# Optimization experiments

Hardware: AMD Instinct MI355X
Metric: run time of the kernel (lower is better)

Reference implementation:

```python
import jax, jax.numpy as jnp
import numpy as np

NEG_INF = -1.0e9


def _gru_cell(x, h, W_ih, W_hh, b_ih, b_hh):
    # torch GRU gate order: reset, update, new
    gi = x @ W_ih.T + b_ih          # [B, 3H]
    gh = h @ W_hh.T + b_hh          # [B, 3H]
    i_r, i_z, i_n = jnp.split(gi, 3, axis=-1)
    h_r, h_z, h_n = jnp.split(gh, 3, axis=-1)
    r = jax.nn.sigmoid(i_r + h_r)
    z = jax.nn.sigmoid(i_z + h_z)
    ng = jnp.tanh(i_n + r * h_n)
    return (1.0 - z) * ng + z * h


def setup_inputs() -> dict:
    key = jax.random.key(0)
    n, H, B = 512, 512, 256
    ks = jax.random.split(key, 10)
    s_ih0 = 1.0 / np.sqrt(n)
    s = 1.0 / np.sqrt(H)
    return {
        "batch_size": B,
        "W_ih0": jax.random.normal(ks[0], (3 * H, n), jnp.float32) * s_ih0,
        "W_hh0": jax.random.normal(ks[1], (3 * H, H), jnp.float32) * s,
        "b_ih0": jax.random.normal(ks[2], (3 * H,), jnp.float32) * s,
        "b_hh0": jax.random.normal(ks[3], (3 * H,), jnp.float32) * s,
        "W_ih1": jax.random.normal(ks[4], (3 * H, H), jnp.float32) * s,
        "W_hh1": jax.random.normal(ks[5], (3 * H, H), jnp.float32) * s,
        "b_ih1": jax.random.normal(ks[6], (3 * H,), jnp.float32) * s,
        "b_hh1": jax.random.normal(ks[7], (3 * H,), jnp.float32) * s,
        "W_out": jax.random.normal(ks[8], (n, H), jnp.float32) * s,
        "b_out": jax.random.normal(ks[9], (n,), jnp.float32) * s,
    }


def reference(batch_size, W_ih0, W_hh0, b_ih0, b_hh0,
              W_ih1, W_hh1, b_ih1, b_hh1, W_out, b_out):
    n = W_out.shape[0]
    H = W_out.shape[1]
    B = batch_size

    h0 = jnp.zeros((B, H), jnp.float32)
    h1 = jnp.zeros((B, H), jnp.float32)
    available = jnp.ones((B, n), jnp.bool_)
    inp = jnp.ones((B, n), jnp.float32)
    log_probs = jnp.zeros((B,), jnp.float32)

    step_keys = jax.random.split(jax.random.key(42), n)

    def step(carry, key):
        h0, h1, available, inp, lp = carry
        h0n = _gru_cell(inp, h0, W_ih0, W_hh0, b_ih0, b_hh0)
        h1n = _gru_cell(h0n, h1, W_ih1, W_hh1, b_ih1, b_hh1)
        logits = h1n @ W_out.T + b_out                       # [B, n]
        logits = jnp.where(available, logits, NEG_INF)
        probs = jax.nn.softmax(logits, axis=-1)
        idx = jax.random.categorical(key, logits, axis=-1)   # ~ multinomial(probs)
        p_sel = jnp.take_along_axis(probs, idx[:, None], axis=1)[:, 0]
        lp = lp + jnp.log(p_sel + 1e-9)
        oh = jax.nn.one_hot(idx, n, dtype=jnp.float32)       # row of perm matrix
        available = available & ~jax.nn.one_hot(idx, n, dtype=jnp.bool_)
        return (h0n, h1n, available, oh, lp), oh

    (h0, h1, available, inp, log_probs), rows = jax.lax.scan(
        step, (h0, h1, available, inp, log_probs), step_keys)
    perm_matrix = jnp.transpose(rows, (1, 0, 2))             # [B, n, n]
    return perm_matrix, log_probs
```

## Files before the change

### kernel.cpp

```cpp
#include <hip/hip_runtime.h>
#include <cstdint>
#include <cstddef>

#define BB 256
#define NN 512
#define HH 512
#define G3 1536

typedef short bf16x8 __attribute__((ext_vector_type(8)));
typedef float f32x4 __attribute__((ext_vector_type(4)));

__device__ __align__(16) short g_Whh0[2 * 786432];
__device__ __align__(16) short g_Whh1[2 * 786432];
__device__ __align__(16) short g_Wih1[2 * 786432];
__device__ __align__(16) short g_Wout[2 * 262144];
__device__ __align__(16) short g_h0p[2][2 * 131072];
__device__ __align__(16) short g_h1p[2][2 * 131072];
__device__ __align__(16) float g_h0f[BB * HH];
__device__ __align__(16) float g_h1f[BB * HH];
__device__ __align__(16) float g_gh1[BB * G3];
__device__ __align__(16) float g_logits[2][BB * NN];
__device__ __align__(16) float g_gum[2][BB * NN];
__device__ __align__(16) float g_WihT[NN * G3];
__device__ __align__(16) float g_ones[G3];
__device__ float g_lp[BB];
__device__ unsigned g_avail[2][BB * 16];
__device__ int g_idx[BB];

__device__ __forceinline__ unsigned short bf16_rne(float f) {
  uint32_t u = __float_as_uint(f);
  uint32_t r = u + 0x7FFFu + ((u >> 16) & 1u);
  return (unsigned short)(r >> 16);
}
__device__ __forceinline__ float bf16_to_f(unsigned short h) {
  return __uint_as_float(((uint32_t)h) << 16);
}
__device__ __forceinline__ float sigf(float x) {
  return 1.0f / (1.0f + expf(-x));
}
__device__ __forceinline__ f32x4 mfma16(bf16x8 a, bf16x8 b, f32x4 c) {
  return __builtin_amdgcn_mfma_f32_16x16x32_bf16(a, b, c, 0, 0, 0);
}

__device__ __forceinline__ uint32_t rotl32(uint32_t v, int r) {
  return (v << r) | (v >> (32 - r));
}
__device__ __forceinline__ void threefry2x32(uint32_t k0, uint32_t k1,
                                             uint32_t x0, uint32_t x1,
                                             uint32_t& o0, uint32_t& o1) {
  uint32_t k2 = k0 ^ k1 ^ 0x1BD11BDAu;
  x0 += k0; x1 += k1;
  x0 += x1; x1 = rotl32(x1, 13); x1 ^= x0;
  x0 += x1; x1 = rotl32(x1, 15); x1 ^= x0;
  x0 += x1; x1 = rotl32(x1, 26); x1 ^= x0;
  x0 += x1; x1 = rotl32(x1, 6);  x1 ^= x0;
  x0 += k1; x1 += k2 + 1u;
  x0 += x1; x1 = rotl32(x1, 17); x1 ^= x0;
  x0 += x1; x1 = rotl32(x1, 29); x1 ^= x0;
  x0 += x1; x1 = rotl32(x1, 16); x1 ^= x0;
  x0 += x1; x1 = rotl32(x1, 24); x1 ^= x0;
  x0 += k2; x1 += k0 + 2u;
  x0 += x1; x1 = rotl32(x1, 13); x1 ^= x0;
  x0 += x1; x1 = rotl32(x1, 15); x1 ^= x0;
  x0 += x1; x1 = rotl32(x1, 26); x1 ^= x0;
  x0 += x1; x1 = rotl32(x1, 6);  x1 ^= x0;
  x0 += k0; x1 += k1 + 3u;
  x0 += x1; x1 = rotl32(x1, 17); x1 ^= x0;
  x0 += x1; x1 = rotl32(x1, 29); x1 ^= x0;
  x0 += x1; x1 = rotl32(x1, 16); x1 ^= x0;
  x0 += x1; x1 = rotl32(x1, 24); x1 ^= x0;
  x0 += k1; x1 += k2 + 4u;
  x0 += x1; x1 = rotl32(x1, 13); x1 ^= x0;
  x0 += x1; x1 = rotl32(x1, 15); x1 ^= x0;
  x0 += x1; x1 = rotl32(x1, 26); x1 ^= x0;
  x0 += x1; x1 = rotl32(x1, 6);  x1 ^= x0;
  x0 += k2; x1 += k0 + 5u;
  o0 = x0; o1 = x1;
}

__device__ __forceinline__ float gumbel_from_bits(uint32_t bits) {
  float u = __uint_as_float((bits >> 9) | 0x3f800000u) - 1.0f;
  if (u == 0.0f) u = 1.17549435e-38f;
  return -logf(-logf(u));
}

__global__ __launch_bounds__(256) void init_state_kernel() {
  int i = blockIdx.x * 256 + threadIdx.x;
  if (i < BB * HH) { g_h0f[i] = 0.0f; g_h1f[i] = 0.0f; }
  if (i < 262144) {
    ((uint32_t*)g_h0p)[i] = 0u;
    ((uint32_t*)g_h1p)[i] = 0u;
  }
  if (i < 2 * BB * 16) ((unsigned*)g_avail)[i] = 0xFFFFFFFFu;
  if (i < BB) { g_lp[i] = 0.0f; g_idx[i] = 0; }
}

__global__ __launch_bounds__(256) void ones_row_kernel(
    const float* __restrict__ W_ih0, const float* __restrict__ b_ih0) {
  int j = blockIdx.x * 256 + threadIdx.x;
  if (j < G3) {
    const float* row = W_ih0 + (size_t)j * NN;
    float s = 0.0f;
    for (int k = 0; k < NN; ++k) s += row[k];
    g_ones[j] = s + b_ih0[j];
  }
}

__global__ __launch_bounds__(256) void transpose_kernel(
    const float* __restrict__ in) {
  __shared__ float tile[32][33];
  int bx = blockIdx.x;
  int by = blockIdx.y;
  int tx = threadIdx.x & 31;
  int ty = threadIdx.x >> 5;
  for (int i = 0; i < 32; i += 8)
    tile[ty + i][tx] = in[(size_t)(by * 32 + ty + i) * NN + bx * 32 + tx];
  __syncthreads();
  for (int i = 0; i < 32; i += 8)
    g_WihT[(size_t)(bx * 32 + ty + i) * G3 + by * 32 + tx] = tile[tx][ty + i];
}

__global__ __launch_bounds__(256) void split_kernel(
    const float* __restrict__ W, short* __restrict__ dst, int rows,
    int plane) {
  int i = blockIdx.x * 256 + threadIdx.x;
  if (i >= rows * 64) return;
  int c = i >> 6;
  int jb = i & 63;
  int ci = c & 15;
  int tile = (rows == G3) ? (((c & 511) >> 4) * 3 + (c >> 9)) : (c >> 4);
  int S = jb >> 2, qu = jb & 3;
  int off = (tile * 16 + S) * 512 + qu * 128 + ci * 8;
  const float* src = W + (size_t)c * 512 + jb * 8;
  float v[8];
  *(float4*)v = *(const float4*)src;
  *(float4*)(v + 4) = *(const float4*)(src + 4);
  short hb[8], lb[8];
#pragma unroll
  for (int e = 0; e < 8; ++e) {
    unsigned short h = bf16_rne(v[e]);
    hb[e] = (short)h;
    lb[e] = (short)bf16_rne(v[e] - bf16_to_f(h));
  }
  *(bf16x8*)(dst + off) = *(const bf16x8*)hb;
  *(bf16x8*)(dst + plane + off) = *(const bf16x8*)lb;
}

__global__ __launch_bounds__(256) void k0_sample(
    int t, const float* __restrict__ b_out, float* __restrict__ out_perm,
    float* __restrict__ out_lp) {
  const int mt = blockIdx.x;
  const int tid = threadIdx.x;
  if (t < NN) {
    float* lz = g_logits[t & 1] + mt * 16 * NN;
    for (int i = tid; i < 16 * NN; i += 256) lz[i] = 0.0f;
  }
  if (t == 0) return;
  const int tp = t - 1;
  const int rr = tid >> 4, l16 = tid & 15;
  const int b = mt * 16 + rr;
  const float* lrow = g_logits[tp & 1] + b * NN;
  const float* grow = g_gum[tp & 1] + b * NN;
  unsigned aw = g_avail[tp & 1][b * 16 + l16];

  float best = -1.0f / 0.0f;
  int bi = 0;
  float sum = 0.0f;
  for (int k = 0; k < 32; ++k) {
    int c = l16 * 32 + k;
    float l = lrow[c] + b_out[c];
    bool av = (aw >> k) & 1u;
    float ml = av ? l : -1.0e9f;
    float v = grow[c] + ml;
    if (v > best || (v == best && c < bi)) { best = v; bi = c; }
    sum += av ? expf(l) : 0.0f;
  }
  __shared__ float sv[256];
  __shared__ int si[256];
  __shared__ float ss[256];
  sv[tid] = best; si[tid] = bi; ss[tid] = sum;
  __syncthreads();
  for (int s = 8; s > 0; s >>= 1) {
    if (l16 < s) {
      float v2 = sv[tid + s]; int i2 = si[tid + s];
      if (v2 > sv[tid] || (v2 == sv[tid] && i2 < si[tid])) {
        sv[tid] = v2; si[tid] = i2;
      }
      ss[tid] += ss[tid + s];
    }
    __syncthreads();
  }
  const int sel = si[rr * 16];
  const float ssum = ss[rr * 16];
  unsigned nw = aw;
  if ((sel >> 5) == l16) nw &= ~(1u << (sel & 31));
  g_avail[t & 1][b * 16 + l16] = nw;
  if (l16 == 0) {
    float lsel = lrow[sel] + b_out[sel];
    float p = expf(lsel) / ssum;
    float lpn = g_lp[b] + logf(p + 1e-9f);
    g_lp[b] = lpn;
    out_lp[b] = lpn;
    g_idx[b] = sel;
    out_perm[(size_t)b * NN * NN + (size_t)tp * NN + sel] = 1.0f;
  }
}

__global__ __launch_bounds__(256) void k1_layer0(
    int t, const float* __restrict__ b_ih0, const float* __restrict__ b_hh0,
    const float* __restrict__ b_hh1, const float* __restrict__ b_out,
    float* __restrict__ out_perm, float* __restrict__ out_lp) {
  const int bid = blockIdx.x;
  const int mt = bid >> 4, nb = bid & 15;
  const int tid = threadIdx.x;

  {
    float* lz = g_logits[t & 1];
    const int e0 = tid, e1 = tid + 256;
    lz[(mt * 16 + (e0 >> 5)) * NN + nb * 32 + (e0 & 31)] = 0.0f;
    lz[(mt * 16 + (e1 >> 5)) * NN + nb * 32 + (e1 & 31)] = 0.0f;
  }

  __shared__ float sv[256];
  __shared__ int si[256];
  __shared__ float ss[256];
  __shared__ int sel16[16];

  if (t > 0 && nb < 8) {
    const int tp = t - 1;
    const int rr = tid >> 4, l16 = tid & 15;
    const int b = mt * 16 + rr;
    const float* lrow = g_logits[tp & 1] + b * NN;
    const float* grow = g_gum[tp & 1] + b * NN;
    unsigned aw = g_avail[tp & 1][b * 16 + l16];

    float best = -1.0f / 0.0f;
    int bi = 0;
    float sum = 0.0f;
    for (int k = 0; k < 32; ++k) {
      int c = l16 * 32 + k;
      float l = lrow[c] + b_out[c];
      bool av = (aw >> k) & 1u;
      float ml = av ? l : -1.0e9f;
      float v = grow[c] + ml;
      if (v > best || (v == best && c < bi)) { best = v; bi = c; }
      sum += av ? expf(l) : 0.0f;
    }
    sv[tid] = best; si[tid] = bi; ss[tid] = sum;
    __syncthreads();
    for (int s = 8; s > 0; s >>= 1) {
      if (l16 < s) {
        float v2 = sv[tid + s]; int i2 = si[tid + s];
        if (v2 > sv[tid] || (v2 == sv[tid] && i2 < si[tid])) {
          sv[tid] = v2; si[tid] = i2;
        }
        ss[tid] += ss[tid + s];
      }
      __syncthreads();
    }
    const int sel = si[rr * 16];
    if (l16 == 0) sel16[rr] = sel;
    if (nb == 0) {
      unsigned nw = aw;
      if ((sel >> 5) == l16) nw &= ~(1u << (sel & 31));
      g_avail[t & 1][b * 16 + l16] = nw;
      if (l16 == 0) {
        const float ssum = ss[rr * 16];
        float lsel = lrow[sel] + b_out[sel];
        float p = expf(lsel) / ssum;
        float lpn = g_lp[b] + logf(p + 1e-9f);
        g_lp[b] = lpn;
        out_lp[b] = lpn;
        out_perm[(size_t)b * NN * NN + (size_t)tp * NN + sel] = 1.0f;
      }
    }
    __syncthreads();
  }

  const int w = tid >> 6, ln = tid & 63;
  const int ci = ln & 15, qu = ln >> 4;
  const int lnoff = ln * 8;
  const int rb = t & 1, wb = rb ^ 1;

  f32x4 z = (f32x4){0.f, 0.f, 0.f, 0.f};
  f32x4 acc[3] = {z, z, z};

  const int u = (nb & 7) * 4 + w;
  const short* Ap = (nb < 8) ? g_h0p[rb] : g_h1p[rb];
  const short* Wp = (nb < 8) ? g_Whh0 : g_Whh1;

#pragma unroll
  for (int S = 0; S < 16; ++S) {
    const int aoff = mt * 8192 + S * 512 + lnoff;
    bf16x8 ah = *(const bf16x8*)(Ap + aoff);
    bf16x8 al = *(const bf16x8*)(Ap + 131072 + aoff);
#pragma unroll
    for (int g = 0; g < 3; ++g) {
      const short* wp = Wp + ((u * 3 + g) * 16 + S) * 512 + lnoff;
      bf16x8 bh = *(const bf16x8*)wp;
      bf16x8 bl = *(const bf16x8*)(wp + 786432);
      acc[g] = mfma16(ah, bh, acc[g]);
      acc[g] = mfma16(ah, bl, acc[g]);
      acc[g] = mfma16(al, bh, acc[g]);
    }
  }

  const int h = u * 16 + ci;
  if (nb < 8) {
    const float br = b_hh0[h], bz = b_hh0[HH + h], bn = b_hh0[2 * HH + h];
    const float bi0 = b_ih0[h], bi1 = b_ih0[HH + h], bi2 = b_ih0[2 * HH + h];
#pragma unroll
    for (int r = 0; r < 4; ++r) {
      const int b = mt * 16 + qu * 4 + r;
      float ir, iz, in_;
      if (t == 0) {
        ir = g_ones[h]; iz = g_ones[HH + h]; in_ = g_ones[2 * HH + h];
      } else {
        const float* wr_ = g_WihT + (size_t)sel16[qu * 4 + r] * G3;
        ir = wr_[h] + bi0;
        iz = wr_[HH + h] + bi1;
        in_ = wr_[2 * HH + h] + bi2;
      }
      float rr_ = sigf(ir + acc[0][r] + br);
      float zz = sigf(iz + acc[1][r] + bz);
      float ng = tanhf(in_ + rr_ * (acc[2][r] + bn));
      const int o = b * HH + h;
      float hn = (1.f - zz) * ng + zz * g_h0f[o];
      g_h0f[o] = hn;
      const int off = (b >> 4) * 8192 + (h >> 5) * 512 + ((h >> 3) & 3) * 128 +
                      (b & 15) * 8 + (h & 7);
      unsigned short hi = bf16_rne(hn);
      g_h0p[wb][off] = (short)hi;
      g_h0p[wb][131072 + off] = (short)bf16_rne(hn - bf16_to_f(hi));
    }
  } else {
    const float c0 = b_hh1[h], c1 = b_hh1[HH + h], c2 = b_hh1[2 * HH + h];
#pragma unroll
    for (int r = 0; r < 4; ++r) {
      const int b = mt * 16 + qu * 4 + r;
      float* base = g_gh1 + (size_t)b * G3;
      base[h] = acc[0][r] + c0;
      base[512 + h] = acc[1][r] + c1;
      base[1024 + h] = acc[2][r] + c2;
    }
  }
}

__global__ __launch_bounds__(256) void k2_layer1(
    int t, const float* __restrict__ b_ih1) {
  const int bid = blockIdx.x;
  const int mt = bid >> 3, nb = bid & 7;
  const int tid = threadIdx.x;
  const int w = tid >> 6, ln = tid & 63;
  const int ci = ln & 15, qu = ln >> 4;
  const int lnoff = ln * 8;
  const int wb = (t & 1) ^ 1;

  f32x4 z = (f32x4){0.f, 0.f, 0.f, 0.f};
  f32x4 acc[3] = {z, z, z};
  const int u = nb * 4 + w;

#pragma unroll
  for (int S = 0; S < 16; ++S) {
    const int aoff = mt * 8192 + S * 512 + lnoff;
    bf16x8 ah = *(const bf16x8*)(g_h0p[wb] + aoff);
    bf16x8 al = *(const bf16x8*)(g_h0p[wb] + 131072 + aoff);
#pragma unroll
    for (int g = 0; g < 3; ++g) {
      const short* wp = g_Wih1 + ((u * 3 + g) * 16 + S) * 512 + lnoff;
      bf16x8 bh = *(const bf16x8*)wp;
      bf16x8 bl = *(const bf16x8*)(wp + 786432);
      acc[g] = mfma16(ah, bh, acc[g]);
      acc[g] = mfma16(ah, bl, acc[g]);
      acc[g] = mfma16(al, bh, acc[g]);
    }
  }

  const int h = u * 16 + ci;
  const float bi0 = b_ih1[h], bi1 = b_ih1[HH + h], bi2 = b_ih1[2 * HH + h];
  float hn[4];
#pragma unroll
  for (int r = 0; r < 4; ++r) {
    const int b = mt * 16 + qu * 4 + r;
    const float* base = g_gh1 + (size_t)b * G3;
    float rr_ = sigf(acc[0][r] + bi0 + base[h]);
    float zz = sigf(acc[1][r] + bi1 + base[512 + h]);
    float ng = tanhf(acc[2][r] + bi2 + rr_ * base[1024 + h]);
    const int o = b * HH + h;
    float v = (1.f - zz) * ng + zz * g_h1f[o];
    g_h1f[o] = v;
    hn[r] = v;
    const int off = (b >> 4) * 8192 + (h >> 5) * 512 + ((h >> 3) & 3) * 128 +
                    (b & 15) * 8 + (h & 7);
    unsigned short hi = bf16_rne(v);
    g_h1p[wb][off] = (short)hi;
    g_h1p[wb][131072 + off] = (short)bf16_rne(v - bf16_to_f(hi));
  }

  __shared__ short Lh[1024], Ll[1024];
  const int kk = w * 16 + ci;
#pragma unroll
  for (int r = 0; r < 4; ++r) {
    const int m = qu * 4 + r;
    const int off = (kk >> 5) * 512 + ((kk >> 3) & 3) * 128 + m * 8 + (kk & 7);
    unsigned short hi = bf16_rne(hn[r]);
    Lh[off] = (short)hi;
    Ll[off] = (short)bf16_rne(hn[r] - bf16_to_f(hi));
  }
  __syncthreads();

  f32x4 acc2[8] = {z, z, z, z, z, z, z, z};
#pragma unroll
  for (int S2 = 0; S2 < 2; ++S2) {
    bf16x8 ah = *(const bf16x8*)&Lh[S2 * 512 + lnoff];
    bf16x8 al = *(const bf16x8*)&Ll[S2 * 512 + lnoff];
#pragma unroll
    for (int j = 0; j < 8; ++j) {
      const int nt = w * 8 + j;
      const short* wp = g_Wout + (nt * 16 + nb * 2 + S2) * 512 + lnoff;
      bf16x8 bh = *(const bf16x8*)wp;
      bf16x8 bl = *(const bf16x8*)(wp + 262144);
      acc2[j] = mfma16(ah, bh, acc2[j]);
      acc2[j] = mfma16(ah, bl, acc2[j]);
      acc2[j] = mfma16(al, bh, acc2[j]);
    }
  }
  float* Ldst = g_logits[t & 1];
#pragma unroll
  for (int j = 0; j < 8; ++j) {
    const int n = (w * 8 + j) * 16 + ci;
#pragma unroll
    for (int r = 0; r < 4; ++r) {
      const int b = mt * 16 + qu * 4 + r;
      atomicAdd(&Ldst[b * NN + n], acc2[j][r]);
    }
  }

  if (mt < 8) {
    uint32_t tp_ = (uint32_t)(t & 255);
    uint32_t a0, a1, c0, c1;
    threefry2x32(0u, 42u, 2u * tp_, 2u * tp_ + 512u, a0, a1);
    threefry2x32(0u, 42u, 2u * tp_ + 1u, 2u * tp_ + 1u + 512u, c0, c1);
    uint32_t sk0 = (t < 256) ? a0 : a1;
    uint32_t sk1 = (t < 256) ? c0 : c1;
    float* G = g_gum[t & 1];
    for (int e = tid; e < 1024; e += 256) {
      const int r16 = e >> 6;
      const int c = nb * 64 + (e & 63);
      const int b = mt * 16 + r16;
      uint32_t cnt = (uint32_t)b * 512u + (uint32_t)c;
      uint32_t r0, r1;
      threefry2x32(sk0, sk1, cnt, cnt + 65536u, r0, r1);
      G[b * NN + c] = gumbel_from_bits(r0);
      G[(b + 128) * NN + c] = gumbel_from_bits(r1);
    }
  }
}

extern "C" void kernel_launch(void* const* d_in, const int* in_sizes, int n_in,
                              void* d_out, int out_size, void* d_ws,
                              size_t ws_size, hipStream_t stream) {
  (void)in_sizes; (void)n_in; (void)d_ws; (void)ws_size;
  const float* W_ih0 = (const float*)d_in[1];
  const float* W_hh0 = (const float*)d_in[2];
  const float* b_ih0 = (const float*)d_in[3];
  const float* b_hh0 = (const float*)d_in[4];
  const float* W_ih1 = (const float*)d_in[5];
  const float* W_hh1 = (const float*)d_in[6];
  const float* b_ih1 = (const float*)d_in[7];
  const float* b_hh1 = (const float*)d_in[8];
  const float* W_out = (const float*)d_in[9];
  const float* b_out = (const float*)d_in[10];

  float* out = (float*)d_out;
  float* out_lp = out + (size_t)BB * NN * NN;

  hipMemsetAsync(d_out, 0, (size_t)out_size * sizeof(float), stream);
  init_state_kernel<<<1024, 256, 0, stream>>>();
  ones_row_kernel<<<6, 256, 0, stream>>>(W_ih0, b_ih0);
  transpose_kernel<<<dim3(16, 48), 256, 0, stream>>>(W_ih0);

  short* whh0; hipGetSymbolAddress((void**)&whh0, HIP_SYMBOL(g_Whh0));
  short* whh1; hipGetSymbolAddress((void**)&whh1, HIP_SYMBOL(g_Whh1));
  short* wih1; hipGetSymbolAddress((void**)&wih1, HIP_SYMBOL(g_Wih1));
  short* wout; hipGetSymbolAddress((void**)&wout, HIP_SYMBOL(g_Wout));
  split_kernel<<<384, 256, 0, stream>>>(W_hh0, whh0, G3, 786432);
  split_kernel<<<384, 256, 0, stream>>>(W_hh1, whh1, G3, 786432);
  split_kernel<<<384, 256, 0, stream>>>(W_ih1, wih1, G3, 786432);
  split_kernel<<<128, 256, 0, stream>>>(W_out, wout, NN, 262144);

  for (int t = 0; t < NN; ++t) {
    k1_layer0<<<256, 256, 0, stream>>>(t, b_ih0, b_hh0, b_hh1, b_out, out,
                                       out_lp);
    k2_layer1<<<128, 256, 0, stream>>>(t, b_ih1);
  }
  k0_sample<<<16, 256, 0, stream>>>(NN, b_out, out, out_lp);
}
```

Measured before the change: 27.09 ms.

## Split K across two thread halves in GRU kernels and move Gumbel generation

Both per-step kernels now launch 512 threads per block. The two halves each compute half of the K reduction for the recurrent matmuls and combine their partial results through shared memory, which shortens the serial MFMA chain per wave and adds more waves to hide latency. The argmax and softmax-sum reduction now uses 16-lane shuffles instead of shared-memory passes with block barriers. Gumbel noise generation moves from k2 into the idle layer-1 blocks of k1, and the W_out matmul in k2 is divided between the two halves. In exchange there is an extra barrier and shared-memory traffic per kernel, and the nonlinearity stage runs with half the threads idle.

```diff
diff --git a/kernel.cpp b/kernel.cpp
--- a/kernel.cpp
+++ b/kernel.cpp
@@ -206,27 +206,25 @@
   }
 }
 
-__global__ __launch_bounds__(256) void k1_layer0(
+__global__ __launch_bounds__(512) void k1_layer0(
     int t, const float* __restrict__ b_ih0, const float* __restrict__ b_hh0,
     const float* __restrict__ b_hh1, const float* __restrict__ b_out,
     float* __restrict__ out_perm, float* __restrict__ out_lp) {
   const int bid = blockIdx.x;
   const int mt = bid >> 4, nb = bid & 15;
   const int tid = threadIdx.x;
+  const int half = tid >> 8;
+  const int t8 = tid & 255;
+
+  __shared__ int sel16[16];
+  __shared__ float accsh[3][4][256];
 
   {
     float* lz = g_logits[t & 1];
-    const int e0 = tid, e1 = tid + 256;
-    lz[(mt * 16 + (e0 >> 5)) * NN + nb * 32 + (e0 & 31)] = 0.0f;
-    lz[(mt * 16 + (e1 >> 5)) * NN + nb * 32 + (e1 & 31)] = 0.0f;
-  }
-
-  __shared__ float sv[256];
-  __shared__ int si[256];
-  __shared__ float ss[256];
-  __shared__ int sel16[16];
-
-  if (t > 0 && nb < 8) {
+    lz[(mt * 16 + (tid >> 5)) * NN + nb * 32 + (tid & 31)] = 0.0f;
+  }
+
+  if (t > 0 && nb < 8 && tid < 256) {
     const int tp = t - 1;
     const int rr = tid >> 4, l16 = tid & 15;
     const int b = mt * 16 + rr;
@@ -246,38 +244,31 @@
       if (v > best || (v == best && c < bi)) { best = v; bi = c; }
       sum += av ? expf(l) : 0.0f;
     }
-    sv[tid] = best; si[tid] = bi; ss[tid] = sum;
-    __syncthreads();
+#pragma unroll
     for (int s = 8; s > 0; s >>= 1) {
-      if (l16 < s) {
-        float v2 = sv[tid + s]; int i2 = si[tid + s];
-        if (v2 > sv[tid] || (v2 == sv[tid] && i2 < si[tid])) {
-          sv[tid] = v2; si[tid] = i2;
-        }
-        ss[tid] += ss[tid + s];
-      }
-      __syncthreads();
-    }
-    const int sel = si[rr * 16];
-    if (l16 == 0) sel16[rr] = sel;
+      float ov = __shfl_xor(best, s, 16);
+      int oi = __shfl_xor(bi, s, 16);
+      float os = __shfl_xor(sum, s, 16);
+      if (ov > best || (ov == best && oi < bi)) { best = ov; bi = oi; }
+      sum += os;
+    }
+    if (l16 == 0) sel16[rr] = bi;
     if (nb == 0) {
       unsigned nw = aw;
-      if ((sel >> 5) == l16) nw &= ~(1u << (sel & 31));
+      if ((bi >> 5) == l16) nw &= ~(1u << (bi & 31));
       g_avail[t & 1][b * 16 + l16] = nw;
       if (l16 == 0) {
-        const float ssum = ss[rr * 16];
-        float lsel = lrow[sel] + b_out[sel];
-        float p = expf(lsel) / ssum;
+        float lsel = lrow[bi] + b_out[bi];
+        float p = expf(lsel) / sum;
         float lpn = g_lp[b] + logf(p + 1e-9f);
         g_lp[b] = lpn;
         out_lp[b] = lpn;
-        out_perm[(size_t)b * NN * NN + (size_t)tp * NN + sel] = 1.0f;
+        out_perm[(size_t)b * NN * NN + (size_t)tp * NN + bi] = 1.0f;
       }
     }
-    __syncthreads();
-  }
-
-  const int w = tid >> 6, ln = tid & 63;
+  }
+
+  const int w = t8 >> 6, ln = t8 & 63;
   const int ci = ln & 15, qu = ln >> 4;
   const int lnoff = ln * 8;
   const int rb = t & 1, wb = rb ^ 1;
@@ -288,9 +279,11 @@
   const int u = (nb & 7) * 4 + w;
   const short* Ap = (nb < 8) ? g_h0p[rb] : g_h1p[rb];
   const short* Wp = (nb < 8) ? g_Whh0 : g_Whh1;
-
-#pragma unroll
-  for (int S = 0; S < 16; ++S) {
+  const int Sbeg = half * 8;
+
+#pragma unroll
+  for (int So = 0; So < 8; ++So) {
+    const int S = Sbeg + So;
     const int aoff = mt * 8192 + S * 512 + lnoff;
     bf16x8 ah = *(const bf16x8*)(Ap + aoff);
     bf16x8 al = *(const bf16x8*)(Ap + 131072 + aoff);
@@ -305,63 +298,106 @@
     }
   }
 
-  const int h = u * 16 + ci;
-  if (nb < 8) {
-    const float br = b_hh0[h], bz = b_hh0[HH + h], bn = b_hh0[2 * HH + h];
-    const float bi0 = b_ih0[h], bi1 = b_ih0[HH + h], bi2 = b_ih0[2 * HH + h];
-#pragma unroll
-    for (int r = 0; r < 4; ++r) {
-      const int b = mt * 16 + qu * 4 + r;
-      float ir, iz, in_;
-      if (t == 0) {
-        ir = g_ones[h]; iz = g_ones[HH + h]; in_ = g_ones[2 * HH + h];
-      } else {
-        const float* wr_ = g_WihT + (size_t)sel16[qu * 4 + r] * G3;
-        ir = wr_[h] + bi0;
-        iz = wr_[HH + h] + bi1;
-        in_ = wr_[2 * HH + h] + bi2;
+  if (half == 1) {
+#pragma unroll
+    for (int g = 0; g < 3; ++g)
+#pragma unroll
+      for (int r = 0; r < 4; ++r) accsh[g][r][t8] = acc[g][r];
+  }
+  __syncthreads();
+
+  if (tid < 256) {
+#pragma unroll
+    for (int g = 0; g < 3; ++g)
+#pragma unroll
+      for (int r = 0; r < 4; ++r) acc[g][r] += accsh[g][r][t8];
+
+    const int h = u * 16 + ci;
+    if (nb < 8) {
+      const float br = b_hh0[h], bz = b_hh0[HH + h], bn = b_hh0[2 * HH + h];
+      const float bi0 = b_ih0[h], bi1 = b_ih0[HH + h], bi2 = b_ih0[2 * HH + h];
+#pragma unroll
+      for (int r = 0; r < 4; ++r) {
+        const int b = mt * 16 + qu * 4 + r;
+        float ir, iz, in_;
+        if (t == 0) {
+          ir = g_ones[h]; iz = g_ones[HH + h]; in_ = g_ones[2 * HH + h];
+        } else {
+          const float* wr_ = g_WihT + (size_t)sel16[qu * 4 + r] * G3;
+          ir = wr_[h] + bi0;
+          iz = wr_[HH + h] + bi1;
+          in_ = wr_[2 * HH + h] + bi2;
+        }
+        float rr_ = sigf(ir + acc[0][r] + br);
+        float zz = sigf(iz + acc[1][r] + bz);
+        float ng = tanhf(in_ + rr_ * (acc[2][r] + bn));
+        const int o = b * HH + h;
+        float hn = (1.f - zz) * ng + zz * g_h0f[o];
+        g_h0f[o] = hn;
+        const int off = (b >> 4) * 8192 + (h >> 5) * 512 +
+                        ((h >> 3) & 3) * 128 + (b & 15) * 8 + (h & 7);
+        unsigned short hi = bf16_rne(hn);
+        g_h0p[wb][off] = (short)hi;
+        g_h0p[wb][131072 + off] = (short)bf16_rne(hn - bf16_to_f(hi));
       }
-      float rr_ = sigf(ir + acc[0][r] + br);
-      float zz = sigf(iz + acc[1][r] + bz);
-      float ng = tanhf(in_ + rr_ * (acc[2][r] + bn));
-      const int o = b * HH + h;
-      float hn = (1.f - zz) * ng + zz * g_h0f[o];
-      g_h0f[o] = hn;
-      const int off = (b >> 4) * 8192 + (h >> 5) * 512 + ((h >> 3) & 3) * 128 +
-                      (b & 15) * 8 + (h & 7);
-      unsigned short hi = bf16_rne(hn);
-      g_h0p[wb][off] = (short)hi;
-      g_h0p[wb][131072 + off] = (short)bf16_rne(hn - bf16_to_f(hi));
-    }
-  } else {
-    const float c0 = b_hh1[h], c1 = b_hh1[HH + h], c2 = b_hh1[2 * HH + h];
-#pragma unroll
-    for (int r = 0; r < 4; ++r) {
-      const int b = mt * 16 + qu * 4 + r;
-      float* base = g_gh1 + (size_t)b * G3;
-      base[h] = acc[0][r] + c0;
-      base[512 + h] = acc[1][r] + c1;
-      base[1024 + h] = acc[2][r] + c2;
-    }
-  }
-}
-
-__global__ __launch_bounds__(256) void k2_layer1(
+    } else {
+      const float c0 = b_hh1[h], c1 = b_hh1[HH + h], c2 = b_hh1[2 * HH + h];
+#pragma unroll
+      for (int r = 0; r < 4; ++r) {
+        const int b = mt * 16 + qu * 4 + r;
+        float* base = g_gh1 + (size_t)b * G3;
+        base[h] = acc[0][r] + c0;
+        base[512 + h] = acc[1][r] + c1;
+        base[1024 + h] = acc[2][r] + c2;
+      }
+    }
+  }
+
+  if (nb >= 8 && mt < 8) {
+    const int nb2 = nb & 7;
+    uint32_t tp_ = (uint32_t)(t & 255);
+    uint32_t a0, a1, c0, c1;
+    threefry2x32(0u, 42u, 2u * tp_, 2u * tp_ + 512u, a0, a1);
+    threefry2x32(0u, 42u, 2u * tp_ + 1u, 2u * tp_ + 1u + 512u, c0, c1);
+    uint32_t sk0 = (t < 256) ? a0 : a1;
+    uint32_t sk1 = (t < 256) ? c0 : c1;
+    float* G = g_gum[t & 1];
+    for (int e = tid; e < 1024; e += 512) {
+      const int r16 = e >> 6;
+      const int c = nb2 * 64 + (e & 63);
+      const int b = mt * 16 + r16;
+      uint32_t cnt = (uint32_t)b * 512u + (uint32_t)c;
+      uint32_t r0, r1;
+      threefry2x32(sk0, sk1, cnt, cnt + 65536u, r0, r1);
+      G[b * NN + c] = gumbel_from_bits(r0);
+      G[(b + 128) * NN + c] = gumbel_from_bits(r1);
+    }
+  }
+}
+
+__global__ __launch_bounds__(512) void k2_layer1(
     int t, const float* __restrict__ b_ih1) {
   const int bid = blockIdx.x;
   const int mt = bid >> 3, nb = bid & 7;
   const int tid = threadIdx.x;
-  const int w = tid >> 6, ln = tid & 63;
+  const int half = tid >> 8;
+  const int t8 = tid & 255;
+  const int w = t8 >> 6, ln = t8 & 63;
   const int ci = ln & 15, qu = ln >> 4;
   const int lnoff = ln * 8;
   const int wb = (t & 1) ^ 1;
 
+  __shared__ float accsh[3][4][256];
+  __shared__ short Lh[1024], Ll[1024];
+
   f32x4 z = (f32x4){0.f, 0.f, 0.f, 0.f};
   f32x4 acc[3] = {z, z, z};
   const int u = nb * 4 + w;
-
-#pragma unroll
-  for (int S = 0; S < 16; ++S) {
+  const int Sbeg = half * 8;
+
+#pragma unroll
+  for (int So = 0; So < 8; ++So) {
+    const int S = Sbeg + So;
     const int aoff = mt * 8192 + S * 512 + lnoff;
     bf16x8 ah = *(const bf16x8*)(g_h0p[wb] + aoff);
     bf16x8 al = *(const bf16x8*)(g_h0p[wb] + 131072 + aoff);
@@ -376,83 +412,77 @@
     }
   }
 
-  const int h = u * 16 + ci;
-  const float bi0 = b_ih1[h], bi1 = b_ih1[HH + h], bi2 = b_ih1[2 * HH + h];
-  float hn[4];
-#pragma unroll
-  for (int r = 0; r < 4; ++r) {
-    const int b = mt * 16 + qu * 4 + r;
-    const float* base = g_gh1 + (size_t)b * G3;
-    float rr_ = sigf(acc[0][r] + bi0 + base[h]);
-    float zz = sigf(acc[1][r] + bi1 + base[512 + h]);
-    float ng = tanhf(acc[2][r] + bi2 + rr_ * base[1024 + h]);
-    const int o = b * HH + h;
-    float v = (1.f - zz) * ng + zz * g_h1f[o];
-    g_h1f[o] = v;
-    hn[r] = v;
-    const int off = (b >> 4) * 8192 + (h >> 5) * 512 + ((h >> 3) & 3) * 128 +
-                    (b & 15) * 8 + (h & 7);
-    unsigned short hi = bf16_rne(v);
-    g_h1p[wb][off] = (short)hi;
-    g_h1p[wb][131072 + off] = (short)bf16_rne(v - bf16_to_f(hi));
-  }
-
-  __shared__ short Lh[1024], Ll[1024];
-  const int kk = w * 16 + ci;
-#pragma unroll
-  for (int r = 0; r < 4; ++r) {
-    const int m = qu * 4 + r;
-    const int off = (kk >> 5) * 512 + ((kk >> 3) & 3) * 128 + m * 8 + (kk & 7);
-    unsigned short hi = bf16_rne(hn[r]);
-    Lh[off] = (short)hi;
-    Ll[off] = (short)bf16_rne(hn[r] - bf16_to_f(hi));
+  if (half == 1) {
+#pragma unroll
+    for (int g = 0; g < 3; ++g)
+#pragma unroll
+      for (int r = 0; r < 4; ++r) accsh[g][r][t8] = acc[g][r];
   }
   __syncthreads();
 
-  f32x4 acc2[8] = {z, z, z, z, z, z, z, z};
+  if (tid < 256) {
+#pragma unroll
+    for (int g = 0; g < 3; ++g)
+#pragma unroll
+      for (int r = 0; r < 4; ++r) acc[g][r] += accsh[g][r][t8];
+
+    const int h = u * 16 + ci;
+    const float bi0 = b_ih1[h], bi1 = b_ih1[HH + h], bi2 = b_ih1[2 * HH + h];
+    float hn[4];
+#pragma unroll
+    for (int r = 0; r < 4; ++r) {
+      const int b = mt * 16 + qu * 4 + r;
+      const float* base = g_gh1 + (size_t)b * G3;
+      float rr_ = sigf(acc[0][r] + bi0 + base[h]);
+      float zz = sigf(acc[1][r] + bi1 + base[512 + h]);
+      float ng = tanhf(acc[2][r] + bi2 + rr_ * base[1024 + h]);
+      const int o = b * HH + h;
+      float v = (1.f - zz) * ng + zz * g_h1f[o];
+      g_h1f[o] = v;
+      hn[r] = v;
+      const int off = (b >> 4) * 8192 + (h >> 5) * 512 + ((h >> 3) & 3) * 128 +
+                      (b & 15) * 8 + (h & 7);
+      unsigned short hi = bf16_rne(v);
+      g_h1p[wb][off] = (short)hi;
+      g_h1p[wb][131072 + off] = (short)bf16_rne(v - bf16_to_f(hi));
+    }
+
+    const int kk = w * 16 + ci;
+#pragma unroll
+    for (int r = 0; r < 4; ++r) {
+      const int m = qu * 4 + r;
+      const int off = (kk >> 5) * 512 + ((kk >> 3) & 3) * 128 + m * 8 + (kk & 7);
+      unsigned short hi = bf16_rne(hn[r]);
+      Lh[off] = (short)hi;
+      Ll[off] = (short)bf16_rne(hn[r] - bf16_to_f(hi));
+    }
+  }
+  __syncthreads();
+
+  f32x4 acc2[4] = {z, z, z, z};
 #pragma unroll
   for (int S2 = 0; S2 < 2; ++S2) {
     bf16x8 ah = *(const bf16x8*)&Lh[S2 * 512 + lnoff];
     bf16x8 al = *(const bf16x8*)&Ll[S2 * 512 + lnoff];
 #pragma unroll
-    for (int j = 0; j < 8; ++j) {
-      const int nt = w * 8 + j;
+    for (int jj = 0; jj < 4; ++jj) {
+      const int nt = w * 8 + half * 4 + jj;
       const short* wp = g_Wout + (nt * 16 + nb * 2 + S2) * 512 + lnoff;
       bf16x8 bh = *(const bf16x8*)wp;
       bf16x8 bl = *(const bf16x8*)(wp + 262144);
-      acc2[j] = mfma16(ah, bh, acc2[j]);
-      acc2[j] = mfma16(ah, bl, acc2[j]);
-      acc2[j] = mfma16(al, bh, acc2[j]);
+      acc2[jj] = mfma16(ah, bh, acc2[jj]);
+      acc2[jj] = mfma16(ah, bl, acc2[jj]);
+      acc2[jj] = mfma16(al, bh, acc2[jj]);
     }
   }
   float* Ldst = g_logits[t & 1];
 #pragma unroll
-  for (int j = 0; j < 8; ++j) {
-    const int n = (w * 8 + j) * 16 + ci;
+  for (int jj = 0; jj < 4; ++jj) {
+    const int n = (w * 8 + half * 4 + jj) * 16 + ci;
 #pragma unroll
     for (int r = 0; r < 4; ++r) {
       const int b = mt * 16 + qu * 4 + r;
-      atomicAdd(&Ldst[b * NN + n], acc2[j][r]);
-    }
-  }
-
-  if (mt < 8) {
-    uint32_t tp_ = (uint32_t)(t & 255);
-    uint32_t a0, a1, c0, c1;
-    threefry2x32(0u, 42u, 2u * tp_, 2u * tp_ + 512u, a0, a1);
-    threefry2x32(0u, 42u, 2u * tp_ + 1u, 2u * tp_ + 1u + 512u, c0, c1);
-    uint32_t sk0 = (t < 256) ? a0 : a1;
-    uint32_t sk1 = (t < 256) ? c0 : c1;
-    float* G = g_gum[t & 1];
-    for (int e = tid; e < 1024; e += 256) {
-      const int r16 = e >> 6;
-      const int c = nb * 64 + (e & 63);
-      const int b = mt * 16 + r16;
-      uint32_t cnt = (uint32_t)b * 512u + (uint32_t)c;
-      uint32_t r0, r1;
-      threefry2x32(sk0, sk1, cnt, cnt + 65536u, r0, r1);
-      G[b * NN + c] = gumbel_from_bits(r0);
-      G[(b + 128) * NN + c] = gumbel_from_bits(r1);
+      atomicAdd(&Ldst[b * NN + n], acc2[jj][r]);
     }
   }
 }
@@ -490,9 +520,9 @@
   split_kernel<<<128, 256, 0, stream>>>(W_out, wout, NN, 262144);
 
   for (int t = 0; t < NN; ++t) {
-    k1_layer0<<<256, 256, 0, stream>>>(t, b_ih0, b_hh0, b_hh1, b_out, out,
+    k1_layer0<<<256, 512, 0, stream>>>(t, b_ih0, b_hh0, b_hh1, b_out, out,
                                        out_lp);
-    k2_layer1<<<128, 256, 0, stream>>>(t, b_ih1);
+    k2_layer1<<<128, 512, 0, stream>>>(t, b_ih1);
   }
   k0_sample<<<16, 256, 0, stream>>>(NN, b_out, out, out_lp);
 }
```

Result: no change. 26.92 ms, median of 2 (-0.6%).
